# Performance work log

Hardware: AMD Instinct MI355X
Metric: run time of the kernel (lower is better)

## Reference

```python
import jax, jax.numpy as jnp
import numpy as np

N_SPIKES = 16384
N_UNITS = 256
N_NEIGHB = 128
RANK = 5
NC = 64
NC_OBS = 12
N_CAND = 10  # n_candidates*(n_search+1)+n_explore = 3*3+1
D = RANK * NC_OBS
LOG2PI = 1.8378770664093453


def setup_inputs() -> dict:
    key = jax.random.key(0)
    ks = jax.random.split(key, 8)
    features = jax.random.normal(ks[0], (N_SPIKES, RANK, NC_OBS), dtype=jnp.float32)
    mu = jax.random.normal(ks[1], (N_UNITS, RANK, NC), dtype=jnp.float32)
    # PSD inverse marginal covariances per neighborhood: A A^T / D + I
    A = jax.random.normal(ks[2], (N_NEIGHB, D, D), dtype=jnp.float32)
    Coo_inv = jnp.einsum('nij,nkj->nik', A, A) / D + jnp.eye(D, dtype=jnp.float32)
    # logdet of Coo = -logdet(Coo_inv)
    sign, ld = jnp.linalg.slogdet(Coo_inv)
    Coo_logdet = (-ld).astype(jnp.float32)
    log_proportions = jax.nn.log_softmax(jax.random.normal(ks[3], (N_UNITS,), dtype=jnp.float32))
    noise_log_prop = jnp.float32(-3.0)
    cands = jax.random.randint(ks[4], (N_SPIKES, N_CAND), 0, N_UNITS)
    nid = jax.random.randint(ks[5], (N_SPIKES,), 0, N_NEIGHB)
    # distinct observed channels per neighborhood, sorted
    perm = jnp.argsort(jax.random.uniform(ks[6], (N_NEIGHB, NC)), axis=1)
    obs_ix = jnp.sort(perm[:, :NC_OBS], axis=1)
    return {
        'features': features, 'mu': mu, 'Coo_inv': Coo_inv,
        'Coo_logdet': Coo_logdet, 'log_proportions': log_proportions,
        'noise_log_prop': noise_log_prop, 'cands': cands, 'nid': nid,
        'obs_ix': obs_ix,
    }


def reference(features, mu, Coo_inv, Coo_logdet, log_proportions, noise_log_prop, cands, nid, obs_ix):
    N, R, nco = features.shape
    Nu = mu.shape[0]
    C = cands.shape[1]
    Dd = R * nco
    # --- gather per-spike / per-candidate tables (load_batch) ---
    obs = obs_ix[nid]                                   # (N, nco)
    mu_c = mu[cands]                                    # (N, C, R, NC)
    nu = jnp.take_along_axis(mu_c, obs[:, None, None, :], axis=3)  # (N, C, R, nco)
    Cinv = Coo_inv[nid]                                 # (N, D, D)
    base = Coo_logdet[nid] + Dd * LOG2PI                # (N,)
    # --- truncated Gaussian log-likelihoods (te_batch) ---
    xf = features.reshape(N, Dd)
    xc = xf[:, None, :] - nu.reshape(N, C, Dd)          # (N, C, D)
    y = jnp.einsum('nde,nce->ncd', Cinv, xc)
    mahal = jnp.einsum('ncd,ncd->nc', y, xc)
    ll = log_proportions[cands] - 0.5 * (base[:, None] + mahal)
    yn = jnp.einsum('nde,ne->nd', Cinv, xf)
    mahal_noise = jnp.einsum('nd,nd->n', yn, xf)
    ll_noise = noise_log_prop - 0.5 * (base + mahal_noise)
    logliks = jnp.concatenate([ll, ll_noise[:, None]], axis=1)  # (N, C+1)
    Q = jax.nn.softmax(logliks, axis=1)
    # --- scatter-add sufficient statistics per unit ---
    Qc = Q[:, :C]
    seg = cands.reshape(-1)
    counts = jax.ops.segment_sum(Qc.reshape(-1), seg, num_segments=Nu)
    xw = (Qc[:, :, None] * xf[:, None, :]).reshape(N * C, Dd)
    xsum = jax.ops.segment_sum(xw, seg, num_segments=Nu)
    return jnp.concatenate([counts[:, None], xsum], axis=1)  # (Nu, D+1)
```

## Files before the change

### kernel.cpp

```cpp
#include <hip/hip_runtime.h>

#define N_SPIKES 16384
#define N_UNITS  256
#define N_NEIGHB 128
#define RANK     5
#define NC       64
#define NC_OBS   12
#define N_CAND   10
#define DD       60
#define DD4      15
#define OUT_COLS 61
#define OUT_SIZE (N_UNITS * OUT_COLS)
#define NSB      8
#define SCAP     192
#define CNT_PAD  4
#define CAP      (NSB * SCAP)

__global__ __launch_bounds__(512) void precompute_kernel(
    const float* __restrict__ mu, const float* __restrict__ Coo_inv,
    const int* __restrict__ obs_ix, const float* __restrict__ log_prop,
    float* __restrict__ w_buf, float* __restrict__ b_buf,
    int* __restrict__ gcount)
{
    __shared__ float cinv[DD * DD];
    __shared__ float nu_lds[128 * 61];
    __shared__ float q2_lds[128 * 4];

    const int b   = blockIdx.x;
    const int h   = b >> 1;
    const int ub  = (b & 1) * 128;
    const int tid = threadIdx.x;

    if (tid < 32) gcount[b * 32 + tid] = 0;

    {
        const float4* __restrict__ src = (const float4*)(Coo_inv + h * DD * DD);
        float4* __restrict__ dst = (float4*)cinv;
        for (int i = tid; i < (DD * DD) / 4; i += 512) dst[i] = src[i];
    }

    {
        const int ut  = tid >> 2;
        const int dqt = tid & 3;
        const float* __restrict__ mub = mu + (ub + ut) * (RANK * NC);
#pragma unroll
        for (int j = 0; j < DD4; ++j) {
            const int d  = dqt * DD4 + j;
            const int r  = d / NC_OBS;
            const int jj = d - r * NC_OBS;
            const int ch = obs_ix[h * NC_OBS + jj];
            nu_lds[ut * 61 + d] = mub[r * NC + ch];
        }
    }
    __syncthreads();

    const int lane  = tid & 63;
    const int wave  = tid >> 6;
    const int ug    = wave >> 2;
    const int dq    = __builtin_amdgcn_readfirstlane(wave & 3);
    const int u_loc = ug * 64 + lane;
    const int u     = ub + u_loc;
    const int p     = h * N_UNITS + u;

    float wreg[DD4];
#pragma unroll
    for (int j = 0; j < DD4; ++j) wreg[j] = 0.f;

    const float* __restrict__ Crow_base = cinv + dq * DD4;
    for (int e = 0; e < DD; ++e) {
        const float nu_e = nu_lds[u_loc * 61 + e];
        const float* __restrict__ Crow = Crow_base + e * DD;
#pragma unroll
        for (int j = 0; j < DD4; ++j)
            wreg[j] = fmaf(Crow[j], nu_e, wreg[j]);
    }

    float q2 = 0.f;
#pragma unroll
    for (int j = 0; j < DD4; ++j) q2 += wreg[j] * nu_lds[u_loc * 61 + dq * DD4 + j];
    q2_lds[u_loc * 4 + dq] = q2;

    float* __restrict__ wp = w_buf + p * DD + dq * DD4;
#pragma unroll
    for (int j = 0; j < DD4; ++j) wp[j] = wreg[j];

    __syncthreads();
    if ((wave & 3) == 0) {
        const float q2s = q2_lds[u_loc * 4 + 0] + q2_lds[u_loc * 4 + 1]
                        + q2_lds[u_loc * 4 + 2] + q2_lds[u_loc * 4 + 3];
        b_buf[p] = log_prop[u] - 0.5f * q2s;
    }
}

__global__ __launch_bounds__(1024) void spike_bin_kernel(
    const float* __restrict__ features, const float* __restrict__ noise_lp,
    const int* __restrict__ cands, const int* __restrict__ nid,
    const float* __restrict__ w_buf, const float* __restrict__ b_buf,
    int* __restrict__ gcount, int2* __restrict__ bins)
{
    const int tid  = threadIdx.x;
    const int lane = tid & 63;
    const int wave = tid >> 6;
    const int c    = lane & 15;
    const int s    = lane >> 4;
    const int n    = blockIdx.x * 64 + wave * 4 + s;
    const int sb   = blockIdx.x & (NSB - 1);
    const bool act = (c < N_CAND);
    const int cc   = act ? c : (N_CAND - 1);

    const float4* __restrict__ f4 = (const float4*)features;
    const float4* __restrict__ w4 = (const float4*)w_buf;

    const int   h   = nid[n];
    const float nlp = noise_lp[0];
    const int   uc  = cands[n * N_CAND + cc];
    const int   p   = h * N_UNITS + uc;
    const float bb  = b_buf[p];

    float t = 0.f;
#pragma unroll
    for (int k = 0; k < DD4; ++k) {
        const float4 wv = w4[p * DD4 + k];
        const float4 xv = f4[n * DD4 + k];
        t += wv.x * xv.x + wv.y * xv.y + wv.z * xv.z + wv.w * xv.w;
    }
    float ll = act ? (bb + t) : -3.4e38f;

    float m = ll;
    m = fmaxf(m, __shfl_xor(m, 1, 16));
    m = fmaxf(m, __shfl_xor(m, 2, 16));
    m = fmaxf(m, __shfl_xor(m, 4, 16));
    m = fmaxf(m, __shfl_xor(m, 8, 16));
    m = fmaxf(m, nlp);
    const float e = act ? __expf(ll - m) : 0.f;
    float ssum = e;
    ssum += __shfl_xor(ssum, 1, 16);
    ssum += __shfl_xor(ssum, 2, 16);
    ssum += __shfl_xor(ssum, 4, 16);
    ssum += __shfl_xor(ssum, 8, 16);
    ssum += __expf(nlp - m);
    const float q = e / ssum;

    if (act && q > 0.f) {
        const int bi  = uc * NSB + sb;
        const int pos = atomicAdd(&gcount[bi * CNT_PAD], 1);
        if (pos < SCAP) bins[bi * SCAP + pos] = make_int2(n, __float_as_int(q));
    }
}

__global__ __launch_bounds__(512) void unit_accum_kernel(
    const float* __restrict__ features, const int* __restrict__ gcount,
    const int2* __restrict__ bins, float* __restrict__ out)
{
    __shared__ int2  rec[CAP];
    __shared__ float red[8][OUT_COLS];
    __shared__ int   cnts[NSB];
    __shared__ int   offs[NSB + 1];

    const int u    = blockIdx.x;
    const int tid  = threadIdx.x;
    const int lane = tid & 63;
    const int wave = tid >> 6;

    if (tid < NSB) {
        int c = gcount[(u * NSB + tid) * CNT_PAD];
        cnts[tid] = c < SCAP ? c : SCAP;
    }
    __syncthreads();
    if (tid == 0) {
        int o = 0;
#pragma unroll
        for (int sb = 0; sb < NSB; ++sb) { offs[sb] = o; o += cnts[sb]; }
        offs[NSB] = o;
    }
    __syncthreads();

    {
        const int base = offs[wave];
        const int cnt  = cnts[wave];
        const int2* __restrict__ src = bins + (u * NSB + wave) * SCAP;
        for (int i = lane; i < cnt; i += 64) rec[base + i] = src[i];
    }
    __syncthreads();

    const int total = offs[NSB];
    const int g = tid >> 4;
    const int l = lane & 15;

    const float4* __restrict__ f4 = (const float4*)features;
    float4 a = {0.f, 0.f, 0.f, 0.f};
    float sq = 0.f;

    for (int i = g; i < total; i += 32) {
        const int2 r = rec[i];
        const float q = __int_as_float(r.y);
        if (l < DD4) {
            const float4 xv = f4[r.x * DD4 + l];
            a.x = fmaf(q, xv.x, a.x);
            a.y = fmaf(q, xv.y, a.y);
            a.z = fmaf(q, xv.z, a.z);
            a.w = fmaf(q, xv.w, a.w);
        } else if (l == DD4) {
            sq += q;
        }
    }

    a.x += __shfl_xor(a.x, 16, 64);  a.x += __shfl_xor(a.x, 32, 64);
    a.y += __shfl_xor(a.y, 16, 64);  a.y += __shfl_xor(a.y, 32, 64);
    a.z += __shfl_xor(a.z, 16, 64);  a.z += __shfl_xor(a.z, 32, 64);
    a.w += __shfl_xor(a.w, 16, 64);  a.w += __shfl_xor(a.w, 32, 64);
    sq  += __shfl_xor(sq, 16, 64);   sq  += __shfl_xor(sq, 32, 64);

    if (lane < DD4) {
        red[wave][1 + 4*lane + 0] = a.x;
        red[wave][1 + 4*lane + 1] = a.y;
        red[wave][1 + 4*lane + 2] = a.z;
        red[wave][1 + 4*lane + 3] = a.w;
    } else if (lane == DD4) {
        red[wave][0] = sq;
    }
    __syncthreads();

    if (tid < OUT_COLS) {
        float ssum = 0.f;
#pragma unroll
        for (int w = 0; w < 8; ++w) ssum += red[w][tid];
        out[u * OUT_COLS + tid] = ssum;
    }
}

extern "C" void kernel_launch(void* const* d_in, const int* in_sizes, int n_in,
                              void* d_out, int out_size, void* d_ws, size_t ws_size,
                              hipStream_t stream) {
    const float* features    = (const float*)d_in[0];
    const float* mu          = (const float*)d_in[1];
    const float* Coo_inv     = (const float*)d_in[2];
    const float* log_prop    = (const float*)d_in[4];
    const float* noise_lp    = (const float*)d_in[5];
    const int*   cands       = (const int*)d_in[6];
    const int*   nid         = (const int*)d_in[7];
    const int*   obs_ix      = (const int*)d_in[8];
    float* out = (float*)d_out;

    char* ws = (char*)d_ws;
    float* w_buf  = (float*)ws;
    float* b_buf  = (float*)(ws + 7864320);
    int*   gcount = (int*)(ws + 7995392);
    int2*  bins   = (int2*)(ws + 8028160);

    precompute_kernel<<<256, 512, 0, stream>>>(mu, Coo_inv, obs_ix, log_prop,
                                               w_buf, b_buf, gcount);
    spike_bin_kernel<<<256, 1024, 0, stream>>>(features, noise_lp, cands, nid,
                                               w_buf, b_buf, gcount, bins);
    unit_accum_kernel<<<256, 512, 0, stream>>>(features, gcount, bins, out);
}
```

Baseline: 111.0 us.

## Restructure precompute kernel with padded Cinv tiles and float4 LDS reads

The precompute kernel now runs 512 blocks of 256 threads, each covering 64 units of one neighborhood. It stores Cinv in LDS padded to 64 columns so each wave can read 16-column slices as float4, and writes w_buf with float4 stores. The goal is fewer LDS instructions, wider stores and more blocks for better occupancy, at the cost of reloading Cinv twice as often and doing some wasted work on the padded columns.

```diff
diff --git a/kernel.cpp b/kernel.cpp
--- a/kernel.cpp
+++ b/kernel.cpp
@@ -15,28 +15,32 @@
 #define SCAP     192
 #define CNT_PAD  4
 #define CAP      (NSB * SCAP)
-
-__global__ __launch_bounds__(512) void precompute_kernel(
+#define CPAD     64
+
+__global__ __launch_bounds__(256) void precompute_kernel(
     const float* __restrict__ mu, const float* __restrict__ Coo_inv,
     const int* __restrict__ obs_ix, const float* __restrict__ log_prop,
     float* __restrict__ w_buf, float* __restrict__ b_buf,
     int* __restrict__ gcount)
 {
-    __shared__ float cinv[DD * DD];
-    __shared__ float nu_lds[128 * 61];
-    __shared__ float q2_lds[128 * 4];
+    __shared__ float cinv[DD * CPAD];
+    __shared__ float nu_lds[64 * 61];
+    __shared__ float q2_lds[64 * 4];
 
     const int b   = blockIdx.x;
-    const int h   = b >> 1;
-    const int ub  = (b & 1) * 128;
+    const int h   = b >> 2;
+    const int ub  = (b & 3) * 64;
     const int tid = threadIdx.x;
 
-    if (tid < 32) gcount[b * 32 + tid] = 0;
-
-    {
-        const float4* __restrict__ src = (const float4*)(Coo_inv + h * DD * DD);
-        float4* __restrict__ dst = (float4*)cinv;
-        for (int i = tid; i < (DD * DD) / 4; i += 512) dst[i] = src[i];
+    if (tid < 16) gcount[b * 16 + tid] = 0;
+
+    {
+        const float* __restrict__ src = Coo_inv + h * DD * DD;
+        for (int idx = tid; idx < DD * CPAD; idx += 256) {
+            const int e = idx >> 6;
+            const int c = idx & 63;
+            cinv[idx] = (c < DD) ? src[e * DD + c] : 0.f;
+        }
     }
 
     {
@@ -54,40 +58,66 @@
     }
     __syncthreads();
 
-    const int lane  = tid & 63;
-    const int wave  = tid >> 6;
-    const int ug    = wave >> 2;
-    const int dq    = __builtin_amdgcn_readfirstlane(wave & 3);
-    const int u_loc = ug * 64 + lane;
-    const int u     = ub + u_loc;
-    const int p     = h * N_UNITS + u;
-
-    float wreg[DD4];
-#pragma unroll
-    for (int j = 0; j < DD4; ++j) wreg[j] = 0.f;
-
-    const float* __restrict__ Crow_base = cinv + dq * DD4;
+    const int lane = tid & 63;
+    const int dq   = __builtin_amdgcn_readfirstlane(tid >> 6);
+    const int u    = ub + lane;
+    const int p    = h * N_UNITS + u;
+
+    float wreg[16];
+#pragma unroll
+    for (int j = 0; j < 16; ++j) wreg[j] = 0.f;
+
+    const float* __restrict__ Cslice = cinv + dq * 16;
+#pragma unroll 4
     for (int e = 0; e < DD; ++e) {
-        const float nu_e = nu_lds[u_loc * 61 + e];
-        const float* __restrict__ Crow = Crow_base + e * DD;
-#pragma unroll
-        for (int j = 0; j < DD4; ++j)
-            wreg[j] = fmaf(Crow[j], nu_e, wreg[j]);
+        const float nu_e = nu_lds[lane * 61 + e];
+        const float4* __restrict__ c4 =
+            (const float4*)(Cslice + e * CPAD);
+        const float4 c0 = c4[0], c1 = c4[1], c2 = c4[2], c3 = c4[3];
+        wreg[ 0] = fmaf(c0.x, nu_e, wreg[ 0]);
+        wreg[ 1] = fmaf(c0.y, nu_e, wreg[ 1]);
+        wreg[ 2] = fmaf(c0.z, nu_e, wreg[ 2]);
+        wreg[ 3] = fmaf(c0.w, nu_e, wreg[ 3]);
+        wreg[ 4] = fmaf(c1.x, nu_e, wreg[ 4]);
+        wreg[ 5] = fmaf(c1.y, nu_e, wreg[ 5]);
+        wreg[ 6] = fmaf(c1.z, nu_e, wreg[ 6]);
+        wreg[ 7] = fmaf(c1.w, nu_e, wreg[ 7]);
+        wreg[ 8] = fmaf(c2.x, nu_e, wreg[ 8]);
+        wreg[ 9] = fmaf(c2.y, nu_e, wreg[ 9]);
+        wreg[10] = fmaf(c2.z, nu_e, wreg[10]);
+        wreg[11] = fmaf(c2.w, nu_e, wreg[11]);
+        wreg[12] = fmaf(c3.x, nu_e, wreg[12]);
+        wreg[13] = fmaf(c3.y, nu_e, wreg[13]);
+        wreg[14] = fmaf(c3.z, nu_e, wreg[14]);
+        wreg[15] = fmaf(c3.w, nu_e, wreg[15]);
     }
 
     float q2 = 0.f;
 #pragma unroll
-    for (int j = 0; j < DD4; ++j) q2 += wreg[j] * nu_lds[u_loc * 61 + dq * DD4 + j];
-    q2_lds[u_loc * 4 + dq] = q2;
-
-    float* __restrict__ wp = w_buf + p * DD + dq * DD4;
-#pragma unroll
-    for (int j = 0; j < DD4; ++j) wp[j] = wreg[j];
-
-    __syncthreads();
-    if ((wave & 3) == 0) {
-        const float q2s = q2_lds[u_loc * 4 + 0] + q2_lds[u_loc * 4 + 1]
-                        + q2_lds[u_loc * 4 + 2] + q2_lds[u_loc * 4 + 3];
+    for (int j = 0; j < 16; ++j) {
+        const int c = dq * 16 + j;
+        const float nv = nu_lds[lane * 61 + (c < DD ? c : 0)];
+        q2 += (c < DD) ? wreg[j] * nv : 0.f;
+    }
+    q2_lds[lane * 4 + dq] = q2;
+
+    {
+        float* __restrict__ wp = w_buf + p * DD + dq * 16;
+#pragma unroll
+        for (int k = 0; k < 4; ++k) {
+            if (dq * 16 + k * 4 < DD) {
+                float4 o;
+                o.x = wreg[4*k+0]; o.y = wreg[4*k+1];
+                o.z = wreg[4*k+2]; o.w = wreg[4*k+3];
+                *(float4*)(wp + k * 4) = o;
+            }
+        }
+    }
+
+    __syncthreads();
+    if (dq == 0) {
+        const float q2s = q2_lds[lane * 4 + 0] + q2_lds[lane * 4 + 1]
+                        + q2_lds[lane * 4 + 2] + q2_lds[lane * 4 + 3];
         b_buf[p] = log_prop[u] - 0.5f * q2s;
     }
 }
@@ -248,7 +278,7 @@
     int*   gcount = (int*)(ws + 7995392);
     int2*  bins   = (int2*)(ws + 8028160);
 
-    precompute_kernel<<<256, 512, 0, stream>>>(mu, Coo_inv, obs_ix, log_prop,
+    precompute_kernel<<<512, 256, 0, stream>>>(mu, Coo_inv, obs_ix, log_prop,
                                                w_buf, b_buf, gcount);
     spike_bin_kernel<<<256, 1024, 0, stream>>>(features, noise_lp, cands, nid,
                                                w_buf, b_buf, gcount, bins);
```

New measurement: 110.1 us. No clear change (-0.8%).
